# Performance work log

Measured on AMD Instinct MI355X. Metric: run time of the kernel, lower is better.

Reference implementation:

```python
import jax, jax.numpy as jnp
import numpy as np

N = 50000          # nodes
E_RAND = 1_600_000 # random edges (avg degree 32)
IN = 8             # in_features
OUT = 8            # out_features
B = 16             # batch columns of x
T = 5              # edge types AFTER add_self_loops (type 1 = self loop, 2..5 = original)


def setup_inputs() -> dict:
    key = jax.random.key(0)
    k1, k2, k3, k4, k5, k6 = jax.random.split(key, 6)
    x = jax.random.normal(k1, (N * IN, B), jnp.float32)
    loops = jnp.arange(N, dtype=jnp.int32)
    # self loops prepended (type 1), random edges with types 2..T (original types shifted +1)
    src = jnp.concatenate([loops, jax.random.randint(k2, (E_RAND,), 0, N, jnp.int32)])
    dst = jnp.concatenate([loops, jax.random.randint(k3, (E_RAND,), 0, N, jnp.int32)])
    edge_types = jnp.concatenate([
        jnp.ones(N, jnp.int32),
        jax.random.randint(k4, (E_RAND,), 2, T + 1, jnp.int32),
    ])
    bound = 1.0 / np.sqrt(IN)
    # weight_vector reshaped: expand() maps ext_type = ((e-1)*OUT + i)*IN + j + 1
    W = jax.random.uniform(k5, (T, OUT, IN), jnp.float32, -bound, bound)
    # bias_vector reshaped: expand(OUT, 1) -> per (type, out-row) scalar
    Bv = jax.random.uniform(k6, (T, OUT), jnp.float32, -bound, bound)
    return dict(x=x, W=W, Bv=Bv, src=src, dst=dst, edge_types=edge_types)


def reference(x, W, Bv, src, dst, edge_types):
    T_, OUT_, IN_ = W.shape
    Nn = x.shape[0] // IN_
    xr = x.reshape(Nn, IN_, -1)                 # [N, in, B]
    Wg = W[edge_types - 1]                      # [E, out, in] per-edge weight block gather
    msg = jnp.einsum('eoi,eib->eob', Wg, xr[src])  # [E, out, B]
    y = jax.ops.segment_sum(msg, dst, num_segments=Nn)            # [N, out, B]
    yb = jax.ops.segment_sum(Bv[edge_types - 1], dst, num_segments=Nn)  # [N, out]
    y = y + yb[:, :, None]
    return y.reshape(Nn * OUT_, -1)             # [N*out, B]
```

## Files before the change

kernel.cpp:

```cpp
#include <hip/hip_runtime.h>
#include <hip/hip_fp16.h>

#define N_NODES 50000
#define E_RAND  1600000
#define IN_F    8
#define OUT_F   8
#define BATCH   16
#define T_TYPES 5

#define NB      782
#define CAP     2432
#define CHUNK   6144
#define BIN_BLOCKS  ((E_RAND + CHUNK - 1) / CHUNK)
#define CONV_BLOCKS 1563

#define SG_BLOCKS (NB * 2)
#define LCAP      1408

#define OFF_BCUR   0
#define OFF_XH     4096
#define OFF_BINNED 12804096
#define WS_NEEDED  (OFF_BINNED + (size_t)NB * CAP * 4)

__global__ __launch_bounds__(512)
void zero_kernel(int* __restrict__ p, int n) {
    const int i = blockIdx.x * 512 + threadIdx.x;
    if (i < n) p[i] = 0;
}

__global__ __launch_bounds__(512)
void prep_kernel(const float* __restrict__ x, __half* __restrict__ xh,
                 const int* __restrict__ src, const int* __restrict__ dst,
                 const int* __restrict__ et,
                 int* __restrict__ bcur, int* __restrict__ binned) {
    __shared__ int h[NB];
    __shared__ int rbase[NB];
    if (blockIdx.x < BIN_BLOCKS) {
        for (int i = threadIdx.x; i < NB; i += 512) h[i] = 0;
        __syncthreads();
        const int cbase = blockIdx.x * CHUNK;
#pragma unroll 4
        for (int k = 0; k < CHUNK / 512; ++k) {
            const int e = cbase + k * 512 + threadIdx.x;
            if (e < E_RAND) atomicAdd(&h[dst[N_NODES + e] >> 6], 1);
        }
        __syncthreads();
        for (int i = threadIdx.x; i < NB; i += 512) {
            const int c = h[i];
            rbase[i] = c ? atomicAdd(&bcur[i], c) : 0;
            h[i] = 0;
        }
        __syncthreads();
#pragma unroll 4
        for (int k = 0; k < CHUNK / 512; ++k) {
            const int e = cbase + k * 512 + threadIdx.x;
            if (e < E_RAND) {
                const int ee  = N_NODES + e;
                const int d   = dst[ee];
                const int bkt = d >> 6;
                const int payload = ((((d & 63) << 2) | (et[ee] - 2)) << 16) | src[ee];
                binned[bkt * CAP + rbase[bkt] + atomicAdd(&h[bkt], 1)] = payload;
            }
        }
        return;
    }
    const int b = threadIdx.x & 15;
    const int n = (blockIdx.x - BIN_BLOCKS) * 32 + (threadIdx.x >> 4);
    if (n >= N_NODES) return;
    const float* xp = x + n * (IN_F * BATCH) + b;
    union { __half hh[8]; uint4 u; } pk;
#pragma unroll
    for (int i = 0; i < IN_F; ++i) pk.hh[i] = __float2half(xp[i * BATCH]);
    *(uint4*)(xh + (size_t)n * 128 + b * 8) = pk.u;
}

__device__ __forceinline__ void unpack_add(uint4 v, float* xa) {
    const __half2* hp = (const __half2*)&v;
    float2 f;
    f = __half22float2(hp[0]); xa[0] += f.x; xa[1] += f.y;
    f = __half22float2(hp[1]); xa[2] += f.x; xa[3] += f.y;
    f = __half22float2(hp[2]); xa[4] += f.x; xa[5] += f.y;
    f = __half22float2(hp[3]); xa[6] += f.x; xa[7] += f.y;
}

__global__ __launch_bounds__(256)
void sortgather_kernel(const __half* __restrict__ xh,
                       const float* __restrict__ W,
                       const float* __restrict__ Bv,
                       const int* __restrict__ bcur,
                       const int* __restrict__ binned,
                       float* __restrict__ y) {
    __shared__ int   lsort[LCAP];
    __shared__ int   hist[128];
    __shared__ int   cur[128];
    __shared__ int   segoff[129];
    __shared__ float Wl[T_TYPES * OUT_F * IN_F];
    __shared__ float Bvl[T_TYPES * OUT_F];
    __shared__ int   wtot[2];

    const int bkt  = blockIdx.x >> 1;
    const int hf   = blockIdx.x & 1;
    const int cnt  = bcur[bkt];
    const int base = bkt * CAP;
    const int t    = threadIdx.x;

    for (int i = t; i < 320; i += 256) Wl[i] = W[i];
    if (t >= 192 && t < 232) Bvl[t - 192] = Bv[t - 192];
    if (t < 128) hist[t] = 0;
    __syncthreads();

    for (int i = t; i < cnt; i += 256) {
        const int k = binned[base + i] >> 16;
        if ((k >> 7) == hf) atomicAdd(&hist[k & 127], 1);
    }
    __syncthreads();

    if (t < 128) {
        const int lane = t & 63;
        int inc = hist[t];
#pragma unroll
        for (int d = 1; d < 64; d <<= 1) {
            const int u = __shfl_up(inc, d);
            if (lane >= d) inc += u;
        }
        cur[t] = inc;
        if (lane == 63) wtot[t >> 6] = inc;
    }
    __syncthreads();
    if (t < 128) {
        const int wbase = (t >= 64) ? wtot[0] : 0;
        const int excl  = wbase + cur[t] - hist[t];
        segoff[t] = excl;
        cur[t]    = excl;
        if (t == 127) segoff[128] = wtot[0] + wtot[1];
    }
    __syncthreads();

    for (int i = t; i < cnt; i += 256) {
        const int p = binned[base + i];
        const int k = p >> 16;
        if ((k >> 7) == hf)
            lsort[atomicAdd(&cur[k & 127], 1)] = p & 0xFFFF;
    }
    __syncthreads();

    const int gg   = t >> 4;
    const int b    = t & 15;
    const int boff = b * 8;
    const __half* __restrict__ xb = xh + boff;

#pragma unroll
    for (int half = 0; half < 2; ++half) {
        const int ln = gg + half * 16;
        const int n  = bkt * 64 + hf * 32 + ln;
        if (n >= N_NODES) continue;

        float xs[IN_F];
#pragma unroll
        for (int i = 0; i < IN_F; ++i) xs[i] = 0.f;
        unpack_add(*(const uint4*)(xb + (size_t)n * 128), xs);

        float out[OUT_F];
#pragma unroll
        for (int o = 0; o < OUT_F; ++o) {
            const float4 w0 = ((const float4*)(Wl + o * IN_F))[0];
            const float4 w1 = ((const float4*)(Wl + o * IN_F))[1];
            float a = Bvl[o];
            a = fmaf(w0.x, xs[0], a); a = fmaf(w0.y, xs[1], a);
            a = fmaf(w0.z, xs[2], a); a = fmaf(w0.w, xs[3], a);
            a = fmaf(w1.x, xs[4], a); a = fmaf(w1.y, xs[5], a);
            a = fmaf(w1.z, xs[6], a); a = fmaf(w1.w, xs[7], a);
            out[o] = a;
        }

        const int* sp = segoff + ln * 4;
#pragma unroll
        for (int t4 = 0; t4 < 4; ++t4) {
            const int s0 = sp[t4];
            const int s1 = sp[t4 + 1];
            const int c  = s1 - s0;
            if (c == 0) continue;

            float xa[IN_F];
#pragma unroll
            for (int i = 0; i < IN_F; ++i) xa[i] = 0.f;

            int e = s0;
            for (; e + 4 <= s1; e += 4) {
                const int i0 = lsort[e];
                const int i1 = lsort[e + 1];
                const int i2 = lsort[e + 2];
                const int i3 = lsort[e + 3];
                const uint4 v0 = *(const uint4*)(xb + (size_t)i0 * 128);
                const uint4 v1 = *(const uint4*)(xb + (size_t)i1 * 128);
                const uint4 v2 = *(const uint4*)(xb + (size_t)i2 * 128);
                const uint4 v3 = *(const uint4*)(xb + (size_t)i3 * 128);
                unpack_add(v0, xa);
                unpack_add(v1, xa);
                unpack_add(v2, xa);
                unpack_add(v3, xa);
            }
            if (e < s1) {
                uint4 v = *(const uint4*)(xb + (size_t)lsort[e] * 128);
                for (++e; e < s1; ++e) {
                    const uint4 vn = *(const uint4*)(xb + (size_t)lsort[e] * 128);
                    unpack_add(v, xa);
                    v = vn;
                }
                unpack_add(v, xa);
            }

            const float* Wt = Wl + (t4 + 1) * (OUT_F * IN_F);
            const float* Bt = Bvl + (t4 + 1) * OUT_F;
            const float fc = (float)c;
#pragma unroll
            for (int o = 0; o < OUT_F; ++o) {
                const float4 w0 = ((const float4*)(Wt + o * IN_F))[0];
                const float4 w1 = ((const float4*)(Wt + o * IN_F))[1];
                float a = fmaf(fc, Bt[o], out[o]);
                a = fmaf(w0.x, xa[0], a); a = fmaf(w0.y, xa[1], a);
                a = fmaf(w0.z, xa[2], a); a = fmaf(w0.w, xa[3], a);
                a = fmaf(w1.x, xa[4], a); a = fmaf(w1.y, xa[5], a);
                a = fmaf(w1.z, xa[6], a); a = fmaf(w1.w, xa[7], a);
                out[o] = a;
            }
        }

        float* yp = y + (size_t)n * (OUT_F * BATCH) + b;
#pragma unroll
        for (int o = 0; o < OUT_F; ++o)
            yp[o * BATCH] = out[o];
    }
}

__global__ __launch_bounds__(256)
void selfinit_kernel(const float* __restrict__ x,
                     const float* __restrict__ W,
                     const float* __restrict__ Bv,
                     float* __restrict__ y) {
    const int b = threadIdx.x & (BATCH - 1);
    const int n = blockIdx.x * 16 + (threadIdx.x >> 4);
    if (n >= N_NODES) return;
    float xc[IN_F];
#pragma unroll
    for (int i = 0; i < IN_F; ++i) xc[i] = x[(n * IN_F + i) * BATCH + b];
#pragma unroll
    for (int o = 0; o < OUT_F; ++o) {
        float a = Bv[o];
#pragma unroll
        for (int i = 0; i < IN_F; ++i) a = fmaf(W[o * IN_F + i], xc[i], a);
        y[(n * OUT_F + o) * BATCH + b] = a;
    }
}

__global__ __launch_bounds__(256)
void direct_edge_kernel(const float* __restrict__ x,
                        const float* __restrict__ W,
                        const float* __restrict__ Bv,
                        const int* __restrict__ src,
                        const int* __restrict__ dst,
                        const int* __restrict__ et,
                        float* __restrict__ y) {
    const int tid = blockIdx.x * 256 + threadIdx.x;
    const int eg  = tid >> 4;
    const int b   = tid & (BATCH - 1);
    if (eg >= E_RAND) return;
    const int e  = N_NODES + eg;
    const int s  = src[e];
    const int d  = dst[e];
    const int ti = et[e] - 1;
    const float* __restrict__ Wt = W + ti * (OUT_F * IN_F);
    float xc[IN_F];
#pragma unroll
    for (int i = 0; i < IN_F; ++i) xc[i] = x[(s * IN_F + i) * BATCH + b];
    float* yp = y + (size_t)d * (OUT_F * BATCH) + b;
#pragma unroll
    for (int o = 0; o < OUT_F; ++o) {
        float a = Bv[ti * OUT_F + o];
#pragma unroll
        for (int i = 0; i < IN_F; ++i) a = fmaf(Wt[o * IN_F + i], xc[i], a);
        unsafeAtomicAdd(yp + o * BATCH, a);
    }
}

extern "C" void kernel_launch(void* const* d_in, const int* in_sizes, int n_in,
                              void* d_out, int out_size, void* d_ws, size_t ws_size,
                              hipStream_t stream) {
    const float* x   = (const float*)d_in[0];
    const float* W   = (const float*)d_in[1];
    const float* Bv  = (const float*)d_in[2];
    const int*   src = (const int*)d_in[3];
    const int*   dst = (const int*)d_in[4];
    const int*   et  = (const int*)d_in[5];
    float* y = (float*)d_out;

    char* ws = (char*)d_ws;
    int*    bcur   = (int*)(ws + OFF_BCUR);
    __half* xh     = (__half*)(ws + OFF_XH);
    int*    binned = (int*)(ws + OFF_BINNED);

    if (ws_size >= WS_NEEDED) {
        zero_kernel<<<2, 512, 0, stream>>>(bcur, NB);
        prep_kernel<<<BIN_BLOCKS + CONV_BLOCKS, 512, 0, stream>>>(x, xh, src, dst, et, bcur, binned);
        sortgather_kernel<<<SG_BLOCKS, 256, 0, stream>>>(xh, W, Bv, bcur, binned, y);
    } else {
        selfinit_kernel<<<(N_NODES + 15) / 16, 256, 0, stream>>>(x, W, Bv, y);
        direct_edge_kernel<<<(E_RAND * 16 + 255) / 256, 256, 0, stream>>>(x, W, Bv, src, dst, et, y);
    }
}
```

Baseline: 182.1 us.

## Split gather into quarter-bucket units with atomic work stealing; shrink binning chunks

The gather kernel now splits each 64-node bucket into four 16-node units instead of two halves. A persistent grid of 2048 blocks pulls units from a global atomic counter. The binning pass uses 1024-edge chunks instead of 6144, giving many more blocks. The aim is better load balance and occupancy (smaller LDS footprint, more parallel blocks), at the cost of each bucket's binned list being re-scanned four times instead of twice and more global atomics on bucket counters.

```diff
diff --git a/kernel.cpp b/kernel.cpp
--- a/kernel.cpp
+++ b/kernel.cpp
@@ -10,12 +10,14 @@
 
 #define NB      782
 #define CAP     2432
-#define CHUNK   6144
-#define BIN_BLOCKS  ((E_RAND + CHUNK - 1) / CHUNK)
-#define CONV_BLOCKS 1563
-
-#define SG_BLOCKS (NB * 2)
-#define LCAP      1408
+
+#define CHUNK_P      1024
+#define BIN_BLOCKS_P ((E_RAND + CHUNK_P - 1) / CHUNK_P)
+#define CONV_BLOCKS  1563
+
+#define UNITS   (NB * 4)
+#define QCAP    768
+#define SG_GRID 2048
 
 #define OFF_BCUR   0
 #define OFF_XH     4096
@@ -35,12 +37,12 @@
                  int* __restrict__ bcur, int* __restrict__ binned) {
     __shared__ int h[NB];
     __shared__ int rbase[NB];
-    if (blockIdx.x < BIN_BLOCKS) {
+    if (blockIdx.x < BIN_BLOCKS_P) {
         for (int i = threadIdx.x; i < NB; i += 512) h[i] = 0;
         __syncthreads();
-        const int cbase = blockIdx.x * CHUNK;
-#pragma unroll 4
-        for (int k = 0; k < CHUNK / 512; ++k) {
+        const int cbase = blockIdx.x * CHUNK_P;
+#pragma unroll
+        for (int k = 0; k < CHUNK_P / 512; ++k) {
             const int e = cbase + k * 512 + threadIdx.x;
             if (e < E_RAND) atomicAdd(&h[dst[N_NODES + e] >> 6], 1);
         }
@@ -51,8 +53,8 @@
             h[i] = 0;
         }
         __syncthreads();
-#pragma unroll 4
-        for (int k = 0; k < CHUNK / 512; ++k) {
+#pragma unroll
+        for (int k = 0; k < CHUNK_P / 512; ++k) {
             const int e = cbase + k * 512 + threadIdx.x;
             if (e < E_RAND) {
                 const int ee  = N_NODES + e;
@@ -65,7 +67,7 @@
         return;
     }
     const int b = threadIdx.x & 15;
-    const int n = (blockIdx.x - BIN_BLOCKS) * 32 + (threadIdx.x >> 4);
+    const int n = (blockIdx.x - BIN_BLOCKS_P) * 32 + (threadIdx.x >> 4);
     if (n >= N_NODES) return;
     const float* xp = x + n * (IN_F * BATCH) + b;
     union { __half hh[8]; uint4 u; } pk;
@@ -89,147 +91,146 @@
                        const float* __restrict__ Bv,
                        const int* __restrict__ bcur,
                        const int* __restrict__ binned,
+                       int* __restrict__ steal,
                        float* __restrict__ y) {
-    __shared__ int   lsort[LCAP];
-    __shared__ int   hist[128];
-    __shared__ int   cur[128];
-    __shared__ int   segoff[129];
+    __shared__ int   lsort[QCAP];
+    __shared__ int   hist[64];
+    __shared__ int   cur[64];
+    __shared__ int   segoff[65];
     __shared__ float Wl[T_TYPES * OUT_F * IN_F];
     __shared__ float Bvl[T_TYPES * OUT_F];
-    __shared__ int   wtot[2];
-
-    const int bkt  = blockIdx.x >> 1;
-    const int hf   = blockIdx.x & 1;
-    const int cnt  = bcur[bkt];
-    const int base = bkt * CAP;
-    const int t    = threadIdx.x;
-
+    __shared__ int   su;
+
+    const int t = threadIdx.x;
     for (int i = t; i < 320; i += 256) Wl[i] = W[i];
     if (t >= 192 && t < 232) Bvl[t - 192] = Bv[t - 192];
-    if (t < 128) hist[t] = 0;
-    __syncthreads();
-
-    for (int i = t; i < cnt; i += 256) {
-        const int k = binned[base + i] >> 16;
-        if ((k >> 7) == hf) atomicAdd(&hist[k & 127], 1);
-    }
-    __syncthreads();
-
-    if (t < 128) {
-        const int lane = t & 63;
-        int inc = hist[t];
-#pragma unroll
-        for (int d = 1; d < 64; d <<= 1) {
-            const int u = __shfl_up(inc, d);
-            if (lane >= d) inc += u;
-        }
-        cur[t] = inc;
-        if (lane == 63) wtot[t >> 6] = inc;
-    }
-    __syncthreads();
-    if (t < 128) {
-        const int wbase = (t >= 64) ? wtot[0] : 0;
-        const int excl  = wbase + cur[t] - hist[t];
-        segoff[t] = excl;
-        cur[t]    = excl;
-        if (t == 127) segoff[128] = wtot[0] + wtot[1];
-    }
-    __syncthreads();
-
-    for (int i = t; i < cnt; i += 256) {
-        const int p = binned[base + i];
-        const int k = p >> 16;
-        if ((k >> 7) == hf)
-            lsort[atomicAdd(&cur[k & 127], 1)] = p & 0xFFFF;
-    }
-    __syncthreads();
 
     const int gg   = t >> 4;
     const int b    = t & 15;
     const int boff = b * 8;
     const __half* __restrict__ xb = xh + boff;
 
-#pragma unroll
-    for (int half = 0; half < 2; ++half) {
-        const int ln = gg + half * 16;
-        const int n  = bkt * 64 + hf * 32 + ln;
-        if (n >= N_NODES) continue;
-
-        float xs[IN_F];
-#pragma unroll
-        for (int i = 0; i < IN_F; ++i) xs[i] = 0.f;
-        unpack_add(*(const uint4*)(xb + (size_t)n * 128), xs);
-
-        float out[OUT_F];
-#pragma unroll
-        for (int o = 0; o < OUT_F; ++o) {
-            const float4 w0 = ((const float4*)(Wl + o * IN_F))[0];
-            const float4 w1 = ((const float4*)(Wl + o * IN_F))[1];
-            float a = Bvl[o];
-            a = fmaf(w0.x, xs[0], a); a = fmaf(w0.y, xs[1], a);
-            a = fmaf(w0.z, xs[2], a); a = fmaf(w0.w, xs[3], a);
-            a = fmaf(w1.x, xs[4], a); a = fmaf(w1.y, xs[5], a);
-            a = fmaf(w1.z, xs[6], a); a = fmaf(w1.w, xs[7], a);
-            out[o] = a;
-        }
-
-        const int* sp = segoff + ln * 4;
-#pragma unroll
-        for (int t4 = 0; t4 < 4; ++t4) {
-            const int s0 = sp[t4];
-            const int s1 = sp[t4 + 1];
-            const int c  = s1 - s0;
-            if (c == 0) continue;
-
-            float xa[IN_F];
-#pragma unroll
-            for (int i = 0; i < IN_F; ++i) xa[i] = 0.f;
-
-            int e = s0;
-            for (; e + 4 <= s1; e += 4) {
-                const int i0 = lsort[e];
-                const int i1 = lsort[e + 1];
-                const int i2 = lsort[e + 2];
-                const int i3 = lsort[e + 3];
-                const uint4 v0 = *(const uint4*)(xb + (size_t)i0 * 128);
-                const uint4 v1 = *(const uint4*)(xb + (size_t)i1 * 128);
-                const uint4 v2 = *(const uint4*)(xb + (size_t)i2 * 128);
-                const uint4 v3 = *(const uint4*)(xb + (size_t)i3 * 128);
-                unpack_add(v0, xa);
-                unpack_add(v1, xa);
-                unpack_add(v2, xa);
-                unpack_add(v3, xa);
+    for (;;) {
+        if (t == 0) su = atomicAdd(steal, 1);
+        __syncthreads();
+        const int u = su;
+        if (u >= UNITS) return;
+
+        const int bkt  = u >> 2;
+        const int qf   = u & 3;
+        const int cnt  = bcur[bkt];
+        const int base = bkt * CAP;
+
+        if (t < 64) hist[t] = 0;
+        __syncthreads();
+
+        for (int i = t; i < cnt; i += 256) {
+            const int k = binned[base + i] >> 16;
+            if ((k >> 6) == qf) atomicAdd(&hist[k & 63], 1);
+        }
+        __syncthreads();
+
+        if (t < 64) {
+            int inc = hist[t];
+#pragma unroll
+            for (int d = 1; d < 64; d <<= 1) {
+                const int v = __shfl_up(inc, d);
+                if (t >= d) inc += v;
             }
-            if (e < s1) {
-                uint4 v = *(const uint4*)(xb + (size_t)lsort[e] * 128);
-                for (++e; e < s1; ++e) {
-                    const uint4 vn = *(const uint4*)(xb + (size_t)lsort[e] * 128);
-                    unpack_add(v, xa);
-                    v = vn;
-                }
-                unpack_add(v, xa);
-            }
-
-            const float* Wt = Wl + (t4 + 1) * (OUT_F * IN_F);
-            const float* Bt = Bvl + (t4 + 1) * OUT_F;
-            const float fc = (float)c;
+            const int excl = inc - hist[t];
+            segoff[t] = excl;
+            cur[t]    = excl;
+            if (t == 63) segoff[64] = inc;
+        }
+        __syncthreads();
+
+        for (int i = t; i < cnt; i += 256) {
+            const int p = binned[base + i];
+            const int k = p >> 16;
+            if ((k >> 6) == qf)
+                lsort[atomicAdd(&cur[k & 63], 1)] = p & 0xFFFF;
+        }
+        __syncthreads();
+
+        const int n = bkt * 64 + qf * 16 + gg;
+        if (n < N_NODES) {
+            float xs[IN_F];
+#pragma unroll
+            for (int i = 0; i < IN_F; ++i) xs[i] = 0.f;
+            unpack_add(*(const uint4*)(xb + (size_t)n * 128), xs);
+
+            float out[OUT_F];
 #pragma unroll
             for (int o = 0; o < OUT_F; ++o) {
-                const float4 w0 = ((const float4*)(Wt + o * IN_F))[0];
-                const float4 w1 = ((const float4*)(Wt + o * IN_F))[1];
-                float a = fmaf(fc, Bt[o], out[o]);
-                a = fmaf(w0.x, xa[0], a); a = fmaf(w0.y, xa[1], a);
-                a = fmaf(w0.z, xa[2], a); a = fmaf(w0.w, xa[3], a);
-                a = fmaf(w1.x, xa[4], a); a = fmaf(w1.y, xa[5], a);
-                a = fmaf(w1.z, xa[6], a); a = fmaf(w1.w, xa[7], a);
+                const float4 w0 = ((const float4*)(Wl + o * IN_F))[0];
+                const float4 w1 = ((const float4*)(Wl + o * IN_F))[1];
+                float a = Bvl[o];
+                a = fmaf(w0.x, xs[0], a); a = fmaf(w0.y, xs[1], a);
+                a = fmaf(w0.z, xs[2], a); a = fmaf(w0.w, xs[3], a);
+                a = fmaf(w1.x, xs[4], a); a = fmaf(w1.y, xs[5], a);
+                a = fmaf(w1.z, xs[6], a); a = fmaf(w1.w, xs[7], a);
                 out[o] = a;
             }
-        }
-
-        float* yp = y + (size_t)n * (OUT_F * BATCH) + b;
-#pragma unroll
-        for (int o = 0; o < OUT_F; ++o)
-            yp[o * BATCH] = out[o];
+
+            const int* sp = segoff + gg * 4;
+#pragma unroll
+            for (int t4 = 0; t4 < 4; ++t4) {
+                const int s0 = sp[t4];
+                const int s1 = sp[t4 + 1];
+                const int c  = s1 - s0;
+                if (c == 0) continue;
+
+                float xa[IN_F];
+#pragma unroll
+                for (int i = 0; i < IN_F; ++i) xa[i] = 0.f;
+
+                int e = s0;
+                for (; e + 4 <= s1; e += 4) {
+                    const int i0 = lsort[e];
+                    const int i1 = lsort[e + 1];
+                    const int i2 = lsort[e + 2];
+                    const int i3 = lsort[e + 3];
+                    const uint4 v0 = *(const uint4*)(xb + (size_t)i0 * 128);
+                    const uint4 v1 = *(const uint4*)(xb + (size_t)i1 * 128);
+                    const uint4 v2 = *(const uint4*)(xb + (size_t)i2 * 128);
+                    const uint4 v3 = *(const uint4*)(xb + (size_t)i3 * 128);
+                    unpack_add(v0, xa);
+                    unpack_add(v1, xa);
+                    unpack_add(v2, xa);
+                    unpack_add(v3, xa);
+                }
+                if (e < s1) {
+                    uint4 v = *(const uint4*)(xb + (size_t)lsort[e] * 128);
+                    for (++e; e < s1; ++e) {
+                        const uint4 vn = *(const uint4*)(xb + (size_t)lsort[e] * 128);
+                        unpack_add(v, xa);
+                        v = vn;
+                    }
+                    unpack_add(v, xa);
+                }
+
+                const float* Wt = Wl + (t4 + 1) * (OUT_F * IN_F);
+                const float* Bt = Bvl + (t4 + 1) * OUT_F;
+                const float fc = (float)c;
+#pragma unroll
+                for (int o = 0; o < OUT_F; ++o) {
+                    const float4 w0 = ((const float4*)(Wt + o * IN_F))[0];
+                    const float4 w1 = ((const float4*)(Wt + o * IN_F))[1];
+                    float a = fmaf(fc, Bt[o], out[o]);
+                    a = fmaf(w0.x, xa[0], a); a = fmaf(w0.y, xa[1], a);
+                    a = fmaf(w0.z, xa[2], a); a = fmaf(w0.w, xa[3], a);
+                    a = fmaf(w1.x, xa[4], a); a = fmaf(w1.y, xa[5], a);
+                    a = fmaf(w1.z, xa[6], a); a = fmaf(w1.w, xa[7], a);
+                    out[o] = a;
+                }
+            }
+
+            float* yp = y + (size_t)n * (OUT_F * BATCH) + b;
+#pragma unroll
+            for (int o = 0; o < OUT_F; ++o)
+                yp[o * BATCH] = out[o];
+        }
+        __syncthreads();
     }
 }
 
@@ -296,13 +297,14 @@
 
     char* ws = (char*)d_ws;
     int*    bcur   = (int*)(ws + OFF_BCUR);
+    int*    steal  = bcur + NB;
     __half* xh     = (__half*)(ws + OFF_XH);
     int*    binned = (int*)(ws + OFF_BINNED);
 
     if (ws_size >= WS_NEEDED) {
-        zero_kernel<<<2, 512, 0, stream>>>(bcur, NB);
-        prep_kernel<<<BIN_BLOCKS + CONV_BLOCKS, 512, 0, stream>>>(x, xh, src, dst, et, bcur, binned);
-        sortgather_kernel<<<SG_BLOCKS, 256, 0, stream>>>(xh, W, Bv, bcur, binned, y);
+        zero_kernel<<<2, 512, 0, stream>>>(bcur, NB + 1);
+        prep_kernel<<<BIN_BLOCKS_P + CONV_BLOCKS, 512, 0, stream>>>(x, xh, src, dst, et, bcur, binned);
+        sortgather_kernel<<<SG_GRID, 256, 0, stream>>>(xh, W, Bv, bcur, binned, steal, y);
     } else {
         selfinit_kernel<<<(N_NODES + 15) / 16, 256, 0, stream>>>(x, W, Bv, y);
         direct_edge_kernel<<<(E_RAND * 16 + 255) / 256, 256, 0, stream>>>(x, W, Bv, src, dst, et, y);
```

New measurement: 232.0 us. 27.4% more time.

## Fuse prep, binning and sort-gather into one persistent kernel with grid barriers

Applied to the files above, without the earlier changes.

Merges the fp16 conversion, edge binning and per-bucket sort/gather into a single persistent kernel of 2048 blocks. The phases are separated by software grid barriers built from atomic counters. This removes two kernel launches and the gaps between them, and the binning uses smaller chunks spread over more blocks. In exchange it relies on all 2048 blocks being co-resident, checked through an occupancy query. Spin-waiting at the barriers adds cost and can deadlock if residency does not hold.

```diff
diff --git a/kernel.cpp b/kernel.cpp
--- a/kernel.cpp
+++ b/kernel.cpp
@@ -10,12 +10,17 @@
 
 #define NB      782
 #define CAP     2432
-#define CHUNK   6144
-#define BIN_BLOCKS  ((E_RAND + CHUNK - 1) / CHUNK)
-#define CONV_BLOCKS 1563
-
-#define SG_BLOCKS (NB * 2)
-#define LCAP      1408
+
+#define GRID_F   2048
+#define BLK_F    256
+#define CHUNK_F  1024
+#define BINB_F   ((E_RAND + CHUNK_F - 1) / CHUNK_F)
+#define SG_ACT   (NB * 2)
+#define LCAP     1408
+
+#define CHUNK_NP      6144
+#define BIN_BLOCKS_NP ((E_RAND + CHUNK_NP - 1) / CHUNK_NP)
+#define CONV_BLOCKS   1563
 
 #define OFF_BCUR   0
 #define OFF_XH     4096
@@ -26,6 +31,229 @@
 void zero_kernel(int* __restrict__ p, int n) {
     const int i = blockIdx.x * 512 + threadIdx.x;
     if (i < n) p[i] = 0;
+}
+
+__device__ __forceinline__ void unpack_add(uint4 v, float* xa) {
+    const __half2* hp = (const __half2*)&v;
+    float2 f;
+    f = __half22float2(hp[0]); xa[0] += f.x; xa[1] += f.y;
+    f = __half22float2(hp[1]); xa[2] += f.x; xa[3] += f.y;
+    f = __half22float2(hp[2]); xa[4] += f.x; xa[5] += f.y;
+    f = __half22float2(hp[3]); xa[6] += f.x; xa[7] += f.y;
+}
+
+__device__ __forceinline__ void flagbar(int* __restrict__ ctr, int nblk) {
+    __threadfence();
+    __syncthreads();
+    if (threadIdx.x == 0) {
+        atomicAdd(ctr, 1);
+        while (__hip_atomic_load(ctr, __ATOMIC_ACQUIRE,
+                                 __HIP_MEMORY_SCOPE_AGENT) < nblk) {
+            __builtin_amdgcn_s_sleep(2);
+        }
+    }
+    __syncthreads();
+    __threadfence();
+}
+
+__global__ __launch_bounds__(BLK_F, 8)
+void fused_kernel(const float* __restrict__ x, __half* __restrict__ xh,
+                  const float* __restrict__ W, const float* __restrict__ Bv,
+                  const int* __restrict__ src, const int* __restrict__ dst,
+                  const int* __restrict__ et,
+                  int* __restrict__ bcur, int* __restrict__ binned,
+                  int* __restrict__ syncc,
+                  float* __restrict__ y) {
+    __shared__ int   h[NB];
+    __shared__ int   rbase[NB];
+    __shared__ int   lsort[LCAP];
+    __shared__ int   hist[128];
+    __shared__ int   cur[128];
+    __shared__ int   segoff[129];
+    __shared__ float Wl[T_TYPES * OUT_F * IN_F];
+    __shared__ float Bvl[T_TYPES * OUT_F];
+    __shared__ int   wtot[2];
+
+    const int t   = threadIdx.x;
+    const int bid = blockIdx.x;
+
+    for (int i = t; i < 320; i += BLK_F) Wl[i] = W[i];
+    if (t >= 192 && t < 232) Bvl[t - 192] = Bv[t - 192];
+
+    for (int item = bid * BLK_F + t; item < N_NODES * 16; item += GRID_F * BLK_F) {
+        const int n = item >> 4;
+        const int b = item & 15;
+        const float* xp = x + n * (IN_F * BATCH) + b;
+        union { __half hh[8]; uint4 u; } pk;
+#pragma unroll
+        for (int i = 0; i < IN_F; ++i) pk.hh[i] = __float2half(xp[i * BATCH]);
+        *(uint4*)(xh + (size_t)n * 128 + b * 8) = pk.u;
+    }
+    flagbar(&syncc[0], GRID_F);
+
+    if (bid < BINB_F) {
+        for (int i = t; i < NB; i += BLK_F) h[i] = 0;
+        __syncthreads();
+        const int cbase = bid * CHUNK_F;
+#pragma unroll
+        for (int k = 0; k < CHUNK_F / BLK_F; ++k) {
+            const int e = cbase + k * BLK_F + t;
+            if (e < E_RAND) atomicAdd(&h[dst[N_NODES + e] >> 6], 1);
+        }
+        __syncthreads();
+        for (int i = t; i < NB; i += BLK_F) {
+            const int c = h[i];
+            rbase[i] = c ? atomicAdd(&bcur[i], c) : 0;
+            h[i] = 0;
+        }
+        __syncthreads();
+#pragma unroll
+        for (int k = 0; k < CHUNK_F / BLK_F; ++k) {
+            const int e = cbase + k * BLK_F + t;
+            if (e < E_RAND) {
+                const int ee  = N_NODES + e;
+                const int d   = dst[ee];
+                const int bkt = d >> 6;
+                const int payload = ((((d & 63) << 2) | (et[ee] - 2)) << 16) | src[ee];
+                binned[bkt * CAP + rbase[bkt] + atomicAdd(&h[bkt], 1)] = payload;
+            }
+        }
+    }
+    flagbar(&syncc[1], GRID_F);
+
+    if (bid >= SG_ACT) return;
+
+    const int bkt  = bid >> 1;
+    const int hf   = bid & 1;
+    const int cnt  = __hip_atomic_load(&bcur[bkt], __ATOMIC_RELAXED,
+                                       __HIP_MEMORY_SCOPE_AGENT);
+    const int base = bkt * CAP;
+
+    if (t < 128) hist[t] = 0;
+    __syncthreads();
+
+    for (int i = t; i < cnt; i += BLK_F) {
+        const int k = binned[base + i] >> 16;
+        if ((k >> 7) == hf) atomicAdd(&hist[k & 127], 1);
+    }
+    __syncthreads();
+
+    if (t < 128) {
+        const int lane = t & 63;
+        int inc = hist[t];
+#pragma unroll
+        for (int d = 1; d < 64; d <<= 1) {
+            const int u = __shfl_up(inc, d);
+            if (lane >= d) inc += u;
+        }
+        cur[t] = inc;
+        if (lane == 63) wtot[t >> 6] = inc;
+    }
+    __syncthreads();
+    if (t < 128) {
+        const int wbase = (t >= 64) ? wtot[0] : 0;
+        const int excl  = wbase + cur[t] - hist[t];
+        segoff[t] = excl;
+        cur[t]    = excl;
+        if (t == 127) segoff[128] = wtot[0] + wtot[1];
+    }
+    __syncthreads();
+
+    for (int i = t; i < cnt; i += BLK_F) {
+        const int p = binned[base + i];
+        const int k = p >> 16;
+        if ((k >> 7) == hf)
+            lsort[atomicAdd(&cur[k & 127], 1)] = p & 0xFFFF;
+    }
+    __syncthreads();
+
+    const int gg   = t >> 4;
+    const int b    = t & 15;
+    const int boff = b * 8;
+    const __half* __restrict__ xb = xh + boff;
+
+#pragma unroll
+    for (int half = 0; half < 2; ++half) {
+        const int ln = gg + half * 16;
+        const int n  = bkt * 64 + hf * 32 + ln;
+        if (n >= N_NODES) continue;
+
+        float xs[IN_F];
+#pragma unroll
+        for (int i = 0; i < IN_F; ++i) xs[i] = 0.f;
+        unpack_add(*(const uint4*)(xb + (size_t)n * 128), xs);
+
+        float out[OUT_F];
+#pragma unroll
+        for (int o = 0; o < OUT_F; ++o) {
+            const float4 w0 = ((const float4*)(Wl + o * IN_F))[0];
+            const float4 w1 = ((const float4*)(Wl + o * IN_F))[1];
+            float a = Bvl[o];
+            a = fmaf(w0.x, xs[0], a); a = fmaf(w0.y, xs[1], a);
+            a = fmaf(w0.z, xs[2], a); a = fmaf(w0.w, xs[3], a);
+            a = fmaf(w1.x, xs[4], a); a = fmaf(w1.y, xs[5], a);
+            a = fmaf(w1.z, xs[6], a); a = fmaf(w1.w, xs[7], a);
+            out[o] = a;
+        }
+
+        const int* sp = segoff + ln * 4;
+#pragma unroll
+        for (int t4 = 0; t4 < 4; ++t4) {
+            const int s0 = sp[t4];
+            const int s1 = sp[t4 + 1];
+            const int c  = s1 - s0;
+            if (c == 0) continue;
+
+            float xa[IN_F];
+#pragma unroll
+            for (int i = 0; i < IN_F; ++i) xa[i] = 0.f;
+
+            int e = s0;
+            for (; e + 4 <= s1; e += 4) {
+                const int i0 = lsort[e];
+                const int i1 = lsort[e + 1];
+                const int i2 = lsort[e + 2];
+                const int i3 = lsort[e + 3];
+                const uint4 v0 = *(const uint4*)(xb + (size_t)i0 * 128);
+                const uint4 v1 = *(const uint4*)(xb + (size_t)i1 * 128);
+                const uint4 v2 = *(const uint4*)(xb + (size_t)i2 * 128);
+                const uint4 v3 = *(const uint4*)(xb + (size_t)i3 * 128);
+                unpack_add(v0, xa);
+                unpack_add(v1, xa);
+                unpack_add(v2, xa);
+                unpack_add(v3, xa);
+            }
+            if (e < s1) {
+                uint4 v = *(const uint4*)(xb + (size_t)lsort[e] * 128);
+                for (++e; e < s1; ++e) {
+                    const uint4 vn = *(const uint4*)(xb + (size_t)lsort[e] * 128);
+                    unpack_add(v, xa);
+                    v = vn;
+                }
+                unpack_add(v, xa);
+            }
+
+            const float* Wt = Wl + (t4 + 1) * (OUT_F * IN_F);
+            const float* Bt = Bvl + (t4 + 1) * OUT_F;
+            const float fc = (float)c;
+#pragma unroll
+            for (int o = 0; o < OUT_F; ++o) {
+                const float4 w0 = ((const float4*)(Wt + o * IN_F))[0];
+                const float4 w1 = ((const float4*)(Wt + o * IN_F))[1];
+                float a = fmaf(fc, Bt[o], out[o]);
+                a = fmaf(w0.x, xa[0], a); a = fmaf(w0.y, xa[1], a);
+                a = fmaf(w0.z, xa[2], a); a = fmaf(w0.w, xa[3], a);
+                a = fmaf(w1.x, xa[4], a); a = fmaf(w1.y, xa[5], a);
+                a = fmaf(w1.z, xa[6], a); a = fmaf(w1.w, xa[7], a);
+                out[o] = a;
+            }
+        }
+
+        float* yp = y + (size_t)n * (OUT_F * BATCH) + b;
+#pragma unroll
+        for (int o = 0; o < OUT_F; ++o)
+            yp[o * BATCH] = out[o];
+    }
 }
 
 __global__ __launch_bounds__(512)
@@ -35,12 +263,12 @@
                  int* __restrict__ bcur, int* __restrict__ binned) {
     __shared__ int h[NB];
     __shared__ int rbase[NB];
-    if (blockIdx.x < BIN_BLOCKS) {
+    if (blockIdx.x < BIN_BLOCKS_NP) {
         for (int i = threadIdx.x; i < NB; i += 512) h[i] = 0;
         __syncthreads();
-        const int cbase = blockIdx.x * CHUNK;
+        const int cbase = blockIdx.x * CHUNK_NP;
 #pragma unroll 4
-        for (int k = 0; k < CHUNK / 512; ++k) {
+        for (int k = 0; k < CHUNK_NP / 512; ++k) {
             const int e = cbase + k * 512 + threadIdx.x;
             if (e < E_RAND) atomicAdd(&h[dst[N_NODES + e] >> 6], 1);
         }
@@ -52,7 +280,7 @@
         }
         __syncthreads();
 #pragma unroll 4
-        for (int k = 0; k < CHUNK / 512; ++k) {
+        for (int k = 0; k < CHUNK_NP / 512; ++k) {
             const int e = cbase + k * 512 + threadIdx.x;
             if (e < E_RAND) {
                 const int ee  = N_NODES + e;
@@ -65,22 +293,13 @@
         return;
     }
     const int b = threadIdx.x & 15;
-    const int n = (blockIdx.x - BIN_BLOCKS) * 32 + (threadIdx.x >> 4);
+    const int n = (blockIdx.x - BIN_BLOCKS_NP) * 32 + (threadIdx.x >> 4);
     if (n >= N_NODES) return;
     const float* xp = x + n * (IN_F * BATCH) + b;
     union { __half hh[8]; uint4 u; } pk;
 #pragma unroll
     for (int i = 0; i < IN_F; ++i) pk.hh[i] = __float2half(xp[i * BATCH]);
     *(uint4*)(xh + (size_t)n * 128 + b * 8) = pk.u;
-}
-
-__device__ __forceinline__ void unpack_add(uint4 v, float* xa) {
-    const __half2* hp = (const __half2*)&v;
-    float2 f;
-    f = __half22float2(hp[0]); xa[0] += f.x; xa[1] += f.y;
-    f = __half22float2(hp[1]); xa[2] += f.x; xa[3] += f.y;
-    f = __half22float2(hp[2]); xa[4] += f.x; xa[5] += f.y;
-    f = __half22float2(hp[3]); xa[6] += f.x; xa[7] += f.y;
 }
 
 __global__ __launch_bounds__(256)
@@ -296,13 +515,26 @@
 
     char* ws = (char*)d_ws;
     int*    bcur   = (int*)(ws + OFF_BCUR);
+    int*    syncc  = bcur + NB;
     __half* xh     = (__half*)(ws + OFF_XH);
     int*    binned = (int*)(ws + OFF_BINNED);
 
-    if (ws_size >= WS_NEEDED) {
-        zero_kernel<<<2, 512, 0, stream>>>(bcur, NB);
-        prep_kernel<<<BIN_BLOCKS + CONV_BLOCKS, 512, 0, stream>>>(x, xh, src, dst, et, bcur, binned);
-        sortgather_kernel<<<SG_BLOCKS, 256, 0, stream>>>(xh, W, Bv, bcur, binned, y);
+    static int fused_ok = -1;
+    if (fused_ok < 0) {
+        int nb = 0;
+        hipError_t e = hipOccupancyMaxActiveBlocksPerMultiprocessor(
+            &nb, (const void*)fused_kernel, BLK_F, 0);
+        fused_ok = (e == hipSuccess && nb >= 8) ? 1 : 0;
+    }
+
+    if (ws_size >= WS_NEEDED && fused_ok == 1) {
+        zero_kernel<<<2, 512, 0, stream>>>(bcur, NB + 2);
+        fused_kernel<<<GRID_F, BLK_F, 0, stream>>>(x, xh, W, Bv, src, dst, et,
+                                                   bcur, binned, syncc, y);
+    } else if (ws_size >= WS_NEEDED) {
+        zero_kernel<<<2, 512, 0, stream>>>(bcur, NB + 2);
+        prep_kernel<<<BIN_BLOCKS_NP + CONV_BLOCKS, 512, 0, stream>>>(x, xh, src, dst, et, bcur, binned);
+        sortgather_kernel<<<NB * 2, 256, 0, stream>>>(xh, W, Bv, bcur, binned, y);
     } else {
         selfinit_kernel<<<(N_NODES + 15) / 16, 256, 0, stream>>>(x, W, Bv, y);
         direct_edge_kernel<<<(E_RAND * 16 + 255) / 256, 256, 0, stream>>>(x, W, Bv, src, dst, et, y);
```

Result: no change. 185.4 us (+1.8%).

## Build a global CSR by (dst, type) with count-scan-scatter instead of bucket binning

Applied to the files above, without the earlier changes.

Replaces the coarse 64-node bucket binning and per-block local counting sort with a full global CSR. The new pipeline counts edges per (dst, type) bin with global atomics, runs a multi-kernel prefix scan, then scatters 16-bit src indices into place. The gather kernel just loads its segment offsets and indices, with no in-block histogram or sort. The cost is more kernel launches, 200k-bin global atomics with contention, and an extra pass over src/dst/et in the scatter kernel.

```diff
diff --git a/kernel.cpp b/kernel.cpp
--- a/kernel.cpp
+++ b/kernel.cpp
@@ -9,18 +9,22 @@
 #define T_TYPES 5
 
 #define NB      782
-#define CAP     2432
-#define CHUNK   6144
-#define BIN_BLOCKS  ((E_RAND + CHUNK - 1) / CHUNK)
-#define CONV_BLOCKS 1563
+#define NBIN    (N_NODES * 4)
+
+#define ECHUNK       4096
+#define COUNT_BLOCKS ((E_RAND + ECHUNK - 1) / ECHUNK)
+#define CONV_BLOCKS  1563
 
 #define SG_BLOCKS (NB * 2)
 #define LCAP      1408
 
-#define OFF_BCUR   0
-#define OFF_XH     4096
-#define OFF_BINNED 12804096
-#define WS_NEEDED  (OFF_BINNED + (size_t)NB * CAP * 4)
+#define OFF_CNT  0
+#define OFF_OFF  800000
+#define OFF_CUR  1600004
+#define OFF_AUX  2400004
+#define OFF_XH   2401536
+#define OFF_CSR  15201536
+#define WS_NEEDED 18401536
 
 __global__ __launch_bounds__(512)
 void zero_kernel(int* __restrict__ p, int n) {
@@ -29,49 +33,103 @@
 }
 
 __global__ __launch_bounds__(512)
-void prep_kernel(const float* __restrict__ x, __half* __restrict__ xh,
-                 const int* __restrict__ src, const int* __restrict__ dst,
-                 const int* __restrict__ et,
-                 int* __restrict__ bcur, int* __restrict__ binned) {
-    __shared__ int h[NB];
-    __shared__ int rbase[NB];
-    if (blockIdx.x < BIN_BLOCKS) {
-        for (int i = threadIdx.x; i < NB; i += 512) h[i] = 0;
-        __syncthreads();
-        const int cbase = blockIdx.x * CHUNK;
-#pragma unroll 4
-        for (int k = 0; k < CHUNK / 512; ++k) {
-            const int e = cbase + k * 512 + threadIdx.x;
-            if (e < E_RAND) atomicAdd(&h[dst[N_NODES + e] >> 6], 1);
-        }
-        __syncthreads();
-        for (int i = threadIdx.x; i < NB; i += 512) {
-            const int c = h[i];
-            rbase[i] = c ? atomicAdd(&bcur[i], c) : 0;
-            h[i] = 0;
-        }
-        __syncthreads();
-#pragma unroll 4
-        for (int k = 0; k < CHUNK / 512; ++k) {
+void count_conv_kernel(const float* __restrict__ x, __half* __restrict__ xh,
+                       const int* __restrict__ dst, const int* __restrict__ et,
+                       int* __restrict__ counts) {
+    if (blockIdx.x < COUNT_BLOCKS) {
+        const int cbase = blockIdx.x * ECHUNK;
+#pragma unroll
+        for (int k = 0; k < ECHUNK / 512; ++k) {
             const int e = cbase + k * 512 + threadIdx.x;
             if (e < E_RAND) {
-                const int ee  = N_NODES + e;
-                const int d   = dst[ee];
-                const int bkt = d >> 6;
-                const int payload = ((((d & 63) << 2) | (et[ee] - 2)) << 16) | src[ee];
-                binned[bkt * CAP + rbase[bkt] + atomicAdd(&h[bkt], 1)] = payload;
+                const int ee = N_NODES + e;
+                atomicAdd(&counts[dst[ee] * 4 + (et[ee] - 2)], 1);
             }
         }
         return;
     }
     const int b = threadIdx.x & 15;
-    const int n = (blockIdx.x - BIN_BLOCKS) * 32 + (threadIdx.x >> 4);
+    const int n = (blockIdx.x - COUNT_BLOCKS) * 32 + (threadIdx.x >> 4);
     if (n >= N_NODES) return;
     const float* xp = x + n * (IN_F * BATCH) + b;
     union { __half hh[8]; uint4 u; } pk;
 #pragma unroll
     for (int i = 0; i < IN_F; ++i) pk.hh[i] = __float2half(xp[i * BATCH]);
     *(uint4*)(xh + (size_t)n * 128 + b * 8) = pk.u;
+}
+
+__global__ __launch_bounds__(512)
+void scan_blocks_kernel(int* __restrict__ counts, int* __restrict__ aux) {
+    __shared__ int wsum[8];
+    const int t    = threadIdx.x;
+    const int base = blockIdx.x * 1024;
+    const int i0   = base + 2 * t;
+    const int c0   = (i0     < NBIN) ? counts[i0]     : 0;
+    const int c1   = (i0 + 1 < NBIN) ? counts[i0 + 1] : 0;
+    const int s    = c0 + c1;
+    const int lane = t & 63;
+    int inc = s;
+#pragma unroll
+    for (int d = 1; d < 64; d <<= 1) {
+        const int u = __shfl_up(inc, d);
+        if (lane >= d) inc += u;
+    }
+    if (lane == 63) wsum[t >> 6] = inc;
+    __syncthreads();
+    int wb = 0;
+    for (int w = 0; w < (t >> 6); ++w) wb += wsum[w];
+    const int ex = wb + inc - s;
+    if (i0     < NBIN) counts[i0]     = ex;
+    if (i0 + 1 < NBIN) counts[i0 + 1] = ex + c0;
+    if (t == 511) aux[blockIdx.x] = wb + inc;
+}
+
+__global__ __launch_bounds__(64)
+void scan_aux_kernel(int* __restrict__ aux, int nblk) {
+    const int lane = threadIdx.x;
+    int carry = 0;
+    for (int c = 0; c * 64 < nblk; ++c) {
+        const int idx = c * 64 + lane;
+        const int v = (idx < nblk) ? aux[idx] : 0;
+        int inc = v;
+#pragma unroll
+        for (int d = 1; d < 64; d <<= 1) {
+            const int u = __shfl_up(inc, d);
+            if (lane >= d) inc += u;
+        }
+        if (idx < nblk) aux[idx] = carry + inc - v;
+        carry += __shfl(inc, 63);
+    }
+}
+
+__global__ __launch_bounds__(512)
+void finalize_kernel(const int* __restrict__ counts, const int* __restrict__ aux,
+                     int* __restrict__ offs, int* __restrict__ curs) {
+    const int i = blockIdx.x * 512 + threadIdx.x;
+    if (i < NBIN) {
+        const int v = counts[i] + aux[i >> 10];
+        offs[i] = v;
+        curs[i] = v;
+    } else if (i == NBIN) {
+        offs[i] = E_RAND;
+    }
+}
+
+__global__ __launch_bounds__(512)
+void scatter_kernel(const int* __restrict__ src, const int* __restrict__ dst,
+                    const int* __restrict__ et,
+                    int* __restrict__ curs, unsigned short* __restrict__ csr) {
+    const int cbase = blockIdx.x * ECHUNK;
+#pragma unroll
+    for (int k = 0; k < ECHUNK / 512; ++k) {
+        const int e = cbase + k * 512 + threadIdx.x;
+        if (e < E_RAND) {
+            const int ee  = N_NODES + e;
+            const int bin = dst[ee] * 4 + (et[ee] - 2);
+            const int pos = atomicAdd(&curs[bin], 1);
+            csr[pos] = (unsigned short)src[ee];
+        }
+    }
 }
 
 __device__ __forceinline__ void unpack_add(uint4 v, float* xa) {
@@ -84,64 +142,34 @@
 }
 
 __global__ __launch_bounds__(256)
-void sortgather_kernel(const __half* __restrict__ xh,
-                       const float* __restrict__ W,
-                       const float* __restrict__ Bv,
-                       const int* __restrict__ bcur,
-                       const int* __restrict__ binned,
-                       float* __restrict__ y) {
+void gather_kernel(const __half* __restrict__ xh,
+                   const float* __restrict__ W,
+                   const float* __restrict__ Bv,
+                   const int* __restrict__ offs,
+                   const unsigned short* __restrict__ csr,
+                   float* __restrict__ y) {
     __shared__ int   lsort[LCAP];
-    __shared__ int   hist[128];
-    __shared__ int   cur[128];
     __shared__ int   segoff[129];
     __shared__ float Wl[T_TYPES * OUT_F * IN_F];
     __shared__ float Bvl[T_TYPES * OUT_F];
-    __shared__ int   wtot[2];
-
-    const int bkt  = blockIdx.x >> 1;
-    const int hf   = blockIdx.x & 1;
-    const int cnt  = bcur[bkt];
-    const int base = bkt * CAP;
-    const int t    = threadIdx.x;
+
+    const int bkt = blockIdx.x >> 1;
+    const int hf  = blockIdx.x & 1;
+    const int gb0 = bkt * 256 + hf * 128;
+    const int t   = threadIdx.x;
 
     for (int i = t; i < 320; i += 256) Wl[i] = W[i];
     if (t >= 192 && t < 232) Bvl[t - 192] = Bv[t - 192];
-    if (t < 128) hist[t] = 0;
+    if (t < 129) {
+        const int g = gb0 + t;
+        segoff[t] = offs[g < NBIN ? g : NBIN];
+    }
     __syncthreads();
 
-    for (int i = t; i < cnt; i += 256) {
-        const int k = binned[base + i] >> 16;
-        if ((k >> 7) == hf) atomicAdd(&hist[k & 127], 1);
-    }
-    __syncthreads();
-
-    if (t < 128) {
-        const int lane = t & 63;
-        int inc = hist[t];
-#pragma unroll
-        for (int d = 1; d < 64; d <<= 1) {
-            const int u = __shfl_up(inc, d);
-            if (lane >= d) inc += u;
-        }
-        cur[t] = inc;
-        if (lane == 63) wtot[t >> 6] = inc;
-    }
-    __syncthreads();
-    if (t < 128) {
-        const int wbase = (t >= 64) ? wtot[0] : 0;
-        const int excl  = wbase + cur[t] - hist[t];
-        segoff[t] = excl;
-        cur[t]    = excl;
-        if (t == 127) segoff[128] = wtot[0] + wtot[1];
-    }
-    __syncthreads();
-
-    for (int i = t; i < cnt; i += 256) {
-        const int p = binned[base + i];
-        const int k = p >> 16;
-        if ((k >> 7) == hf)
-            lsort[atomicAdd(&cur[k & 127], 1)] = p & 0xFFFF;
-    }
+    const int off0 = segoff[0];
+    const int cnt  = segoff[128] - off0;
+
+    for (int i = t; i < cnt; i += 256) lsort[i] = (int)csr[off0 + i];
     __syncthreads();
 
     const int gg   = t >> 4;
@@ -176,8 +204,8 @@
         const int* sp = segoff + ln * 4;
 #pragma unroll
         for (int t4 = 0; t4 < 4; ++t4) {
-            const int s0 = sp[t4];
-            const int s1 = sp[t4 + 1];
+            const int s0 = sp[t4] - off0;
+            const int s1 = sp[t4 + 1] - off0;
             const int c  = s1 - s0;
             if (c == 0) continue;
 
@@ -295,14 +323,21 @@
     float* y = (float*)d_out;
 
     char* ws = (char*)d_ws;
-    int*    bcur   = (int*)(ws + OFF_BCUR);
-    __half* xh     = (__half*)(ws + OFF_XH);
-    int*    binned = (int*)(ws + OFF_BINNED);
+    int*            counts = (int*)(ws + OFF_CNT);
+    int*            offs   = (int*)(ws + OFF_OFF);
+    int*            curs   = (int*)(ws + OFF_CUR);
+    int*            aux    = (int*)(ws + OFF_AUX);
+    __half*         xh     = (__half*)(ws + OFF_XH);
+    unsigned short* csr    = (unsigned short*)(ws + OFF_CSR);
 
     if (ws_size >= WS_NEEDED) {
-        zero_kernel<<<2, 512, 0, stream>>>(bcur, NB);
-        prep_kernel<<<BIN_BLOCKS + CONV_BLOCKS, 512, 0, stream>>>(x, xh, src, dst, et, bcur, binned);
-        sortgather_kernel<<<SG_BLOCKS, 256, 0, stream>>>(xh, W, Bv, bcur, binned, y);
+        zero_kernel<<<(NBIN + 511) / 512, 512, 0, stream>>>(counts, NBIN);
+        count_conv_kernel<<<COUNT_BLOCKS + CONV_BLOCKS, 512, 0, stream>>>(x, xh, dst, et, counts);
+        scan_blocks_kernel<<<(NBIN + 1023) / 1024, 512, 0, stream>>>(counts, aux);
+        scan_aux_kernel<<<1, 64, 0, stream>>>(aux, (NBIN + 1023) / 1024);
+        finalize_kernel<<<(NBIN + 512) / 512, 512, 0, stream>>>(counts, aux, offs, curs);
+        scatter_kernel<<<COUNT_BLOCKS, 512, 0, stream>>>(src, dst, et, curs, csr);
+        gather_kernel<<<SG_BLOCKS, 256, 0, stream>>>(xh, W, Bv, offs, csr, y);
     } else {
         selfinit_kernel<<<(N_NODES + 15) / 16, 256, 0, stream>>>(x, W, Bv, y);
         direct_edge_kernel<<<(E_RAND * 16 + 255) / 256, 256, 0, stream>>>(x, W, Bv, src, dst, et, y);
```

Result: slower. 316.2 us (+73.7%).
